# Kernel tuning notes

Measured on AMD Instinct MI355X. Metric: run time of the kernel, lower is better.

## Reference

```python
import jax, jax.numpy as jnp
import numpy as np

B, D_IN, UNITS = 8192, 4096, 4096

def setup_inputs() -> dict:
    key = jax.random.key(0)
    k1, k2 = jax.random.split(key)
    x = jax.random.normal(k1, (B, D_IN), dtype=jnp.float32)
    kernel = jax.random.normal(k2, (D_IN, UNITS), dtype=jnp.float32) * 0.02  # glorot-ish scale
    bias = jnp.zeros((UNITS,), dtype=jnp.float32)
    return {"x": x, "kernel": kernel, "bias": bias}

def reference(x, kernel, bias):
    # BinaryDense: binarize weights via sign, then dense matmul + bias
    kernel_bin = jnp.sign(kernel)                     # [D_IN, UNITS], values in {-1,0,+1}
    out = jnp.matmul(x, kernel_bin) + bias            # [B, UNITS]
    return out
```

## Files before the change

kernel.cpp:

```cpp
#include <hip/hip_runtime.h>
#include <stdint.h>


typedef int int4v __attribute__((ext_vector_type(4)));
typedef int int16v __attribute__((ext_vector_type(16)));

constexpr int M = 8192, N = 4096, K = 4096;
constexpr int BM = 256, BN = 256, BK = 64;
constexpr int NT = K / BK;
constexpr int BANDSZ = 131072;

__device__ __forceinline__ void gload_lds16(const void* g, void* l) {
  __builtin_amdgcn_global_load_lds(
      (const __attribute__((address_space(1))) unsigned int*)g,
      (__attribute__((address_space(3))) unsigned int*)l, 16, 0, 0);
}

#define FENCE asm volatile("" ::: "memory")

__global__ __launch_bounds__(256) void quant_x_kernel(const float* __restrict__ x,
                                                      signed char* __restrict__ xq,
                                                      float* __restrict__ rscale) {
  const int row = blockIdx.x;
  const int t = threadIdx.x;
  const float* xr = x + (size_t)row * K;
  float4 v[4];
  float mx = 0.f;
#pragma unroll
  for (int i = 0; i < 4; ++i) {
    v[i] = *(const float4*)(xr + t * 16 + i * 4);
    mx = fmaxf(mx, fmaxf(fmaxf(fabsf(v[i].x), fabsf(v[i].y)),
                         fmaxf(fabsf(v[i].z), fabsf(v[i].w))));
  }
#pragma unroll
  for (int off = 32; off >= 1; off >>= 1)
    mx = fmaxf(mx, __shfl_xor(mx, off, 64));
  __shared__ float smax[4];
  if ((t & 63) == 0) smax[t >> 6] = mx;
  __syncthreads();
  const float rm = fmaxf(fmaxf(smax[0], smax[1]), fmaxf(smax[2], smax[3]));
  const float s = (rm > 0.f) ? 127.f / rm : 0.f;
  if (t == 0) rscale[row] = (rm > 0.f) ? rm / 127.f : 0.f;
  uint32_t o[4];
#pragma unroll
  for (int i = 0; i < 4; ++i) {
    float f[4] = {v[i].x, v[i].y, v[i].z, v[i].w};
    uint32_t p = 0;
#pragma unroll
    for (int j = 0; j < 4; ++j) {
      int q = (int)rintf(f[j] * s);
      p |= ((uint32_t)(uint8_t)(signed char)q) << (8 * j);
    }
    o[i] = p;
  }
  *(int4v*)(xq + (size_t)row * K + t * 16) = (int4v){(int)o[0], (int)o[1], (int)o[2], (int)o[3]};
}

__global__ __launch_bounds__(256) void prep2_kernel(const float* __restrict__ w,
                                                    signed char* __restrict__ wq,
                                                    signed char* __restrict__ xq) {
  const int t = threadIdx.x;
  if (blockIdx.x < 4096) {
    __shared__ __align__(16) signed char tile[64 * 68];
    const int idx = blockIdx.x;
    const int n0 = (idx & 63) * 64, k0 = (idx >> 6) * 64;
#pragma unroll
    for (int i = 0; i < 4; ++i) {
      int kl = (t >> 4) + i * 16;
      int nl = (t & 15) * 4;
      float4 v = *(const float4*)(w + (size_t)(k0 + kl) * N + n0 + nl);
      uint32_t p = 0;
      p |= ((uint32_t)(uint8_t)(signed char)((v.x > 0.f) - (v.x < 0.f)));
      p |= ((uint32_t)(uint8_t)(signed char)((v.y > 0.f) - (v.y < 0.f))) << 8;
      p |= ((uint32_t)(uint8_t)(signed char)((v.z > 0.f) - (v.z < 0.f))) << 16;
      p |= ((uint32_t)(uint8_t)(signed char)((v.w > 0.f) - (v.w < 0.f))) << 24;
      *(uint32_t*)(tile + kl * 68 + nl) = p;
    }
    __syncthreads();
    const int nl = t >> 2;
    const int ci = t & 3;
    uint32_t o[4] = {0, 0, 0, 0};
#pragma unroll
    for (int j = 0; j < 16; ++j)
      o[j >> 2] |= ((uint32_t)(uint8_t)tile[(ci * 16 + j) * 68 + nl]) << (8 * (j & 3));
    const int n = n0 + nl;
    const int nband = n >> 5, n31 = n & 31;
    const int tt = k0 >> 6;
    *(int4v*)(wq + (size_t)nband * BANDSZ + tt * 2048 + ci * 512 + n31 * 16) =
        (int4v){(int)o[0], (int)o[1], (int)o[2], (int)o[3]};
  } else {
    const int band = blockIdx.x - 4096;
    signed char* base = xq + (size_t)band * BANDSZ;
    const int r31 = t & 31, cp = t >> 5;
    int4v v[32];
#pragma unroll
    for (int g = 0; g < 32; ++g) {
      const int idx = g * 8 + cp;
      v[g] = *(const int4v*)(base + r31 * 4096 + (idx >> 2) * 64 + (idx & 3) * 16);
    }
    __syncthreads();
#pragma unroll
    for (int g = 0; g < 32; ++g) {
      const int idx = g * 8 + cp;
      *(int4v*)(base + idx * 512 + r31 * 16) = v[g];
    }
  }
}


#define RD_SET(AN, BN_, P, KK)                                                 \
  {                                                                            \
    _Pragma("unroll") for (int mi_ = 0; mi_ < 4; ++mi_) {                      \
      AN[mi_] = *(const int4v*)(smem + (P)*32768 + wm * 8192 + mi_ * 2048 +    \
                                (KK)*1024 + lane16);                           \
    }                                                                          \
    _Pragma("unroll") for (int ni_ = 0; ni_ < 2; ++ni_) {                      \
      BN_[ni_] = *(const int4v*)(smem + (P)*32768 + 16384 + wn * 4096 +        \
                                 ni_ * 2048 + (KK)*1024 + lane16);             \
    }                                                                          \
  }

#define MM(AN, BN_)                                                            \
  {                                                                            \
    __builtin_amdgcn_s_setprio(1);                                             \
    _Pragma("unroll") for (int mi_ = 0; mi_ < 4; ++mi_) {                      \
      _Pragma("unroll") for (int ni_ = 0; ni_ < 2; ++ni_) {                    \
        acc[mi_][ni_] = __builtin_amdgcn_mfma_i32_32x32x32_i8(                 \
            AN[mi_], BN_[ni_], acc[mi_][ni_], 0, 0, 0);                        \
      }                                                                        \
    }                                                                          \
    __builtin_amdgcn_s_setprio(0);                                             \
  }

#define TILE(P, Q, S, T)                                                       \
  {                                                                            \
    RD_SET(aY, bY, P, 1);                                                      \
    const bool more2_ = (T) + 2 < NT;                                          \
    if (more2_) stage(S, (T) + 2);                                             \
    MM(aX, bX);                                                                \
    if (more2_) {                                                              \
      asm volatile("s_waitcnt vmcnt(4)" ::: "memory");                         \
    } else {                                                                   \
      asm volatile("s_waitcnt vmcnt(0)" ::: "memory");                         \
    }                                                                          \
    __builtin_amdgcn_s_barrier();                                              \
    FENCE;                                                                     \
    if ((T) + 1 < NT) RD_SET(aX, bX, Q, 0);                                    \
    MM(aY, bY);                                                                \
    FENCE;                                                                     \
  }

__global__ __launch_bounds__(512, 2) void gemm_bin_kernel(
    const signed char* __restrict__ Xq,
    const signed char* __restrict__ Wq,
    const float* __restrict__ rscale,
    const float* __restrict__ bias,
    float* __restrict__ out) {
  __shared__ __align__(16) signed char smem[131072];

  const int tid = threadIdx.x;
  const int w = tid >> 6;
  const int lane = tid & 63;
  const int wm = w >> 2;
  const int wn = w & 3;
  const int hi = lane >> 5;
  const int l31 = lane & 31;
  const int lane16 = lane * 16;
  const size_t m0 = (size_t)blockIdx.y * BM;
  const size_t n0 = (size_t)blockIdx.x * BN;

  int16v acc[4][2];
#pragma unroll
  for (int i = 0; i < 4; ++i)
#pragma unroll
    for (int j = 0; j < 2; ++j)
#pragma unroll
      for (int r = 0; r < 16; ++r) acc[i][j][r] = 0;
  int4v aX[4], bX[2], aY[4], bY[2];

  const size_t abase0 = (m0 >> 5) * (size_t)BANDSZ;
  const size_t bbase0 = (n0 >> 5) * (size_t)BANDSZ;
  auto stage = [&](int pb, int t) {
    signed char* lb = smem + pb * 32768;
    const size_t at = abase0 + (size_t)t * 2048;
    const size_t bt = bbase0 + (size_t)t * 2048;
#pragma unroll
    for (int it = 0; it < 2; ++it) {
      int pos = it * 512 + tid;
      gload_lds16(Xq + at + (size_t)(pos >> 7) * BANDSZ + ((pos >> 6) & 1) * 1024 +
                      (pos & 63) * 16,
                  lb + pos * 16);
    }
#pragma unroll
    for (int it = 0; it < 2; ++it) {
      int pos = it * 512 + tid;
      gload_lds16(Wq + bt + (size_t)(pos >> 7) * BANDSZ + ((pos >> 6) & 1) * 1024 +
                      (pos & 63) * 16,
                  lb + 16384 + pos * 16);
    }
  };

  stage(0, 0);
  stage(1, 1);
  asm volatile("s_waitcnt vmcnt(4)" ::: "memory");
  __builtin_amdgcn_s_barrier();
  FENCE;
  RD_SET(aX, bX, 0, 0);

#pragma unroll 1
  for (int t = 0; t < NT; t += 4) {
    TILE(0, 1, 2, t)
    TILE(1, 2, 3, t + 1)
    TILE(2, 3, 0, t + 2)
    TILE(3, 0, 1, t + 3)
  }

#pragma unroll
  for (int mi = 0; mi < 4; ++mi) {
    const size_t rbase = m0 + wm * 128 + mi * 32;
    float sc[4][4];
#pragma unroll
    for (int q = 0; q < 4; ++q)
      *(float4*)sc[q] = *(const float4*)(rscale + rbase + hi * 4 + q * 8);
#pragma unroll
    for (int ni = 0; ni < 2; ++ni) {
      const size_t col = n0 + wn * 64 + ni * 32 + l31;
      const float bv = bias[col];
#pragma unroll
      for (int r = 0; r < 16; ++r) {
        const int row = (r & 3) + 8 * (r >> 2) + 4 * hi;
        out[(rbase + row) * N + col] = (float)acc[mi][ni][r] * sc[r >> 2][r & 3] + bv;
      }
    }
  }
}

extern "C" void kernel_launch(void* const* d_in, const int* in_sizes, int n_in,
                              void* d_out, int out_size, void* d_ws, size_t ws_size,
                              hipStream_t stream) {
  const float* x = (const float*)d_in[0];
  const float* kern = (const float*)d_in[1];
  const float* bias = (const float*)d_in[2];
  float* out = (float*)d_out;

  signed char* Xq = (signed char*)d_ws;
  signed char* Wq = Xq + (size_t)M * K;
  float* rscale = (float*)(Wq + (size_t)N * K);

  quant_x_kernel<<<M, 256, 0, stream>>>(x, Xq, rscale);
  prep2_kernel<<<4096 + 256, 256, 0, stream>>>(kern, Wq, Xq);
  gemm_bin_kernel<<<dim3(N / BN, M / BM), 512, 0, stream>>>(Xq, Wq, rscale, bias, out);
}
```

Measured before the change: 395.3 us.

## Split x quantization into max pass and fused quantize-permute pass

Row max/scale computation is merged with weight binarization into one kernel. A second kernel re-reads x, quantizes it and writes directly in the banded GEMM layout through a swizzled LDS tile. This removes the separate in-place xq permutation pass, at the cost of reading x twice.

```diff
diff --git a/kernel.cpp b/kernel.cpp
--- a/kernel.cpp
+++ b/kernel.cpp
@@ -18,51 +18,33 @@
 
 #define FENCE asm volatile("" ::: "memory")
 
-__global__ __launch_bounds__(256) void quant_x_kernel(const float* __restrict__ x,
-                                                      signed char* __restrict__ xq,
-                                                      float* __restrict__ rscale) {
-  const int row = blockIdx.x;
+__global__ __launch_bounds__(256) void prepA_kernel(const float* __restrict__ x,
+                                                    float* __restrict__ rscale,
+                                                    float* __restrict__ rsinv,
+                                                    const float* __restrict__ w,
+                                                    signed char* __restrict__ wq) {
   const int t = threadIdx.x;
-  const float* xr = x + (size_t)row * K;
-  float4 v[4];
-  float mx = 0.f;
-#pragma unroll
-  for (int i = 0; i < 4; ++i) {
-    v[i] = *(const float4*)(xr + t * 16 + i * 4);
-    mx = fmaxf(mx, fmaxf(fmaxf(fabsf(v[i].x), fabsf(v[i].y)),
-                         fmaxf(fabsf(v[i].z), fabsf(v[i].w))));
-  }
-#pragma unroll
-  for (int off = 32; off >= 1; off >>= 1)
-    mx = fmaxf(mx, __shfl_xor(mx, off, 64));
-  __shared__ float smax[4];
-  if ((t & 63) == 0) smax[t >> 6] = mx;
-  __syncthreads();
-  const float rm = fmaxf(fmaxf(smax[0], smax[1]), fmaxf(smax[2], smax[3]));
-  const float s = (rm > 0.f) ? 127.f / rm : 0.f;
-  if (t == 0) rscale[row] = (rm > 0.f) ? rm / 127.f : 0.f;
-  uint32_t o[4];
-#pragma unroll
-  for (int i = 0; i < 4; ++i) {
-    float f[4] = {v[i].x, v[i].y, v[i].z, v[i].w};
-    uint32_t p = 0;
-#pragma unroll
-    for (int j = 0; j < 4; ++j) {
-      int q = (int)rintf(f[j] * s);
-      p |= ((uint32_t)(uint8_t)(signed char)q) << (8 * j);
-    }
-    o[i] = p;
-  }
-  *(int4v*)(xq + (size_t)row * K + t * 16) = (int4v){(int)o[0], (int)o[1], (int)o[2], (int)o[3]};
-}
-
-__global__ __launch_bounds__(256) void prep2_kernel(const float* __restrict__ w,
-                                                    signed char* __restrict__ wq,
-                                                    signed char* __restrict__ xq) {
-  const int t = threadIdx.x;
-  if (blockIdx.x < 4096) {
+  if (blockIdx.x < 2048) {
+    const int row = blockIdx.x * 4 + (t >> 6);
+    const int lane = t & 63;
+    const float* xr = x + (size_t)row * K;
+    float mx = 0.f;
+#pragma unroll
+    for (int j = 0; j < 16; ++j) {
+      float4 v = *(const float4*)(xr + j * 256 + lane * 4);
+      mx = fmaxf(mx, fmaxf(fmaxf(fabsf(v.x), fabsf(v.y)),
+                           fmaxf(fabsf(v.z), fabsf(v.w))));
+    }
+#pragma unroll
+    for (int off = 32; off >= 1; off >>= 1)
+      mx = fmaxf(mx, __shfl_xor(mx, off, 64));
+    if (lane == 0) {
+      rscale[row] = (mx > 0.f) ? mx / 127.f : 0.f;
+      rsinv[row] = (mx > 0.f) ? 127.f / mx : 0.f;
+    }
+  } else {
     __shared__ __align__(16) signed char tile[64 * 68];
-    const int idx = blockIdx.x;
+    const int idx = blockIdx.x - 2048;
     const int n0 = (idx & 63) * 64, k0 = (idx >> 6) * 64;
 #pragma unroll
     for (int i = 0; i < 4; ++i) {
@@ -88,22 +70,47 @@
     const int tt = k0 >> 6;
     *(int4v*)(wq + (size_t)nband * BANDSZ + tt * 2048 + ci * 512 + n31 * 16) =
         (int4v){(int)o[0], (int)o[1], (int)o[2], (int)o[3]};
-  } else {
-    const int band = blockIdx.x - 4096;
-    signed char* base = xq + (size_t)band * BANDSZ;
-    const int r31 = t & 31, cp = t >> 5;
-    int4v v[32];
-#pragma unroll
-    for (int g = 0; g < 32; ++g) {
-      const int idx = g * 8 + cp;
-      v[g] = *(const int4v*)(base + r31 * 4096 + (idx >> 2) * 64 + (idx & 3) * 16);
-    }
-    __syncthreads();
-#pragma unroll
-    for (int g = 0; g < 32; ++g) {
-      const int idx = g * 8 + cp;
-      *(int4v*)(base + idx * 512 + r31 * 16) = v[g];
-    }
+  }
+}
+
+__global__ __launch_bounds__(512) void prepB_kernel(const float* __restrict__ x,
+                                                    const float* __restrict__ rsinv,
+                                                    signed char* __restrict__ xq) {
+  __shared__ __align__(16) signed char lq[32 * 2048];
+  const int tid = threadIdx.x;
+  const int band = blockIdx.x >> 1;
+  const int h = blockIdx.x & 1;
+  const int s_ = tid >> 2;
+  const int b_ = tid & 3;
+
+#pragma unroll 4
+  for (int r = 0; r < 32; ++r) {
+    const int row = band * 32 + r;
+    const float s = rsinv[row];
+    float4 v = *(const float4*)(x + (size_t)row * K + h * 2048 + tid * 4);
+    uint32_t p = 0;
+    {
+      int q0 = (int)rintf(v.x * s);
+      int q1 = (int)rintf(v.y * s);
+      int q2 = (int)rintf(v.z * s);
+      int q3 = (int)rintf(v.w * s);
+      p = ((uint32_t)(uint8_t)(signed char)q0) |
+          (((uint32_t)(uint8_t)(signed char)q1) << 8) |
+          (((uint32_t)(uint8_t)(signed char)q2) << 16) |
+          (((uint32_t)(uint8_t)(signed char)q3) << 24);
+    }
+    const int sp = (s_ & 96) | ((s_ ^ r) & 31);
+    *(uint32_t*)(lq + r * 2048 + sp * 16 + b_ * 4) = p;
+  }
+  __syncthreads();
+  const size_t obase = (size_t)band * BANDSZ + (size_t)h * 65536;
+#pragma unroll
+  for (int it = 0; it < 8; ++it) {
+    const int ch = it * 512 + tid;
+    const int ss = ch >> 5, r31 = ch & 31;
+    const int sp = (ss & 96) | ((ss ^ r31) & 31);
+    *(int4v*)(xq + obase + (size_t)ch * 16) =
+        *(const int4v*)(lq + r31 * 2048 + sp * 16);
   }
 }
 
@@ -246,8 +253,9 @@
   signed char* Xq = (signed char*)d_ws;
   signed char* Wq = Xq + (size_t)M * K;
   float* rscale = (float*)(Wq + (size_t)N * K);
-
-  quant_x_kernel<<<M, 256, 0, stream>>>(x, Xq, rscale);
-  prep2_kernel<<<4096 + 256, 256, 0, stream>>>(kern, Wq, Xq);
+  float* rsinv = rscale + M;
+
+  prepA_kernel<<<2048 + 4096, 256, 0, stream>>>(x, rscale, rsinv, kern, Wq);
+  prepB_kernel<<<512, 512, 0, stream>>>(x, rsinv, Xq);
   gemm_bin_kernel<<<dim3(N / BN, M / BM), 512, 0, stream>>>(Xq, Wq, rscale, bias, out);
 }
```

Measured after the change: 411.5 us. 1.04x slower.
